# Performance work log

Measured on AMD Instinct MI355X. Metric: run time of the kernel, lower is better.

The kernel has to match this reference:

```python
import jax, jax.numpy as jnp
import numpy as np

NUM_HEADS = 12
HEAD_DIM = 64  # d_out // num_heads = 768 // 12


def setup_inputs() -> dict:
    key = jax.random.key(0)
    k1, k2 = jax.random.split(key)
    x = jax.random.normal(k1, (2, 2048, 768), dtype=jnp.float32)
    # torch Linear weight: [d_out, d_in], y = x @ W.T
    Wq = jax.random.normal(k2, (768, 768), dtype=jnp.float32) * 0.02
    return {"x": x, "Wq": Wq}


def reference(x, Wq):
    b, n, d_in = x.shape
    H, hd = NUM_HEADS, HEAD_DIM
    d_out = H * hd
    # NOTE: the original module uses Wq for queries, keys AND values.
    qkv = x @ Wq.T                                   # [b, n, d_out]
    h = qkv.reshape(b, n, H, hd).transpose(0, 2, 1, 3)  # [b, H, n, hd]
    scores = jnp.einsum('bhqd,bhkd->bhqk', h, h)      # [b, H, n, n]
    causal = jnp.triu(jnp.ones((n, n), dtype=bool), k=1)
    scores = jnp.where(causal, -jnp.inf, scores)
    attn = jax.nn.softmax(scores / jnp.sqrt(jnp.float32(hd)), axis=-1)
    ctx = jnp.einsum('bhqk,bhkd->bhqd', attn, h)      # [b, H, n, hd]
    # faithful to source: transpose(-2,-1) -> [b, H, hd, n], then view(b, n, d_out)
    ctx = ctx.transpose(0, 1, 3, 2)
    return ctx.reshape(b, n, d_out)
```

## Files before the change

### kernel.cpp

```cpp
#include <hip/hip_runtime.h>
#include <hip/hip_bf16.h>
#include <math.h>

typedef __attribute__((ext_vector_type(8))) short  short8;
typedef __attribute__((ext_vector_type(4))) float  floatx4;

#define MFMA16(a, b, c) __builtin_amdgcn_mfma_f32_16x16x32_bf16(a, b, c, 0, 0, 0)

constexpr int NSEQ = 2048;
constexpr int DIN  = 768;
constexpr int NH   = 12;
constexpr float QSCALE = 0.18033688011112042f;
constexpr int PART_STRIDE = 64 * 64 + 64;
constexpr size_t HB_ELEMS = (size_t)2 * NH * NSEQ * 64;

__device__ __forceinline__ ushort f2bf(float f) {
    unsigned u = __float_as_uint(f);
    u += 0x7FFF + ((u >> 16) & 1);
    return (ushort)(u >> 16);
}
__device__ __forceinline__ float bf2f(ushort u) {
    return __uint_as_float(((unsigned)u) << 16);
}
__device__ __forceinline__ unsigned pk2(float a, float b) {
    __hip_bfloat162 h = __float22bfloat162_rn(float2{a, b});
    return *(unsigned*)&h;
}
__device__ __forceinline__ short8 cvt8(float4 a, float4 b) {
    union { short8 s; unsigned u[4]; } r;
    r.u[0] = pk2(a.x, a.y); r.u[1] = pk2(a.z, a.w);
    r.u[2] = pk2(b.x, b.y); r.u[3] = pk2(b.z, b.w);
    return r.s;
}

__global__ __launch_bounds__(256, 3)
void qkv_mfma(const float* __restrict__ x, const float* __restrict__ Wq,
              ushort* __restrict__ h)
{
    __shared__ ushort As[64 * 72];
    __shared__ ushort Bs[128 * 72];

    const int tid  = threadIdx.x;
    const int w    = tid >> 6;
    const int lane = tid & 63;
    const int m    = lane & 15;
    const int quad = lane >> 4;
    const int r0   = blockIdx.x * 64;
    const int c0   = blockIdx.y * 128;
    const int mrow0 = (w & 1) * 32;
    const int ncol0 = (w >> 1) * 64;

    const int xr = tid >> 2, xc = (tid & 3) * 16;
    const int wr = tid >> 1, wc = (tid & 1) * 32;

    floatx4 C[2][4] = {};
    float4 xa[4], wa[8];

    #pragma unroll
    for (int j = 0; j < 4; ++j)
        xa[j] = *(const float4*)(x + (size_t)(r0 + xr) * DIN + xc + j * 4);
    #pragma unroll
    for (int j = 0; j < 8; ++j)
        wa[j] = *(const float4*)(Wq + (size_t)(c0 + wr) * DIN + wc + j * 4);

    for (int kk = 0; kk < 12; ++kk) {
        __syncthreads();
        *(short8*)&As[xr * 72 + xc]     = cvt8(xa[0], xa[1]);
        *(short8*)&As[xr * 72 + xc + 8] = cvt8(xa[2], xa[3]);
        #pragma unroll
        for (int v = 0; v < 4; ++v)
            *(short8*)&Bs[wr * 72 + wc + v * 8] = cvt8(wa[v * 2], wa[v * 2 + 1]);
        if (kk < 11) {
            const int k0 = (kk + 1) * 64;
            #pragma unroll
            for (int j = 0; j < 4; ++j)
                xa[j] = *(const float4*)(x + (size_t)(r0 + xr) * DIN + k0 + xc + j * 4);
            #pragma unroll
            for (int j = 0; j < 8; ++j)
                wa[j] = *(const float4*)(Wq + (size_t)(c0 + wr) * DIN + k0 + wc + j * 4);
        }
        __syncthreads();

        #pragma unroll
        for (int kt2 = 0; kt2 < 2; ++kt2) {
            short8 a0 = *(const short8*)&As[(mrow0 + m)      * 72 + kt2 * 32 + quad * 8];
            short8 a1 = *(const short8*)&As[(mrow0 + 16 + m) * 72 + kt2 * 32 + quad * 8];
            #pragma unroll
            for (int nt = 0; nt < 4; ++nt) {
                short8 bf = *(const short8*)&Bs[(ncol0 + nt * 16 + m) * 72 + kt2 * 32 + quad * 8];
                C[0][nt] = MFMA16(a0, bf, C[0][nt]);
                C[1][nt] = MFMA16(a1, bf, C[1][nt]);
            }
        }
    }

    #pragma unroll
    for (int mt = 0; mt < 2; ++mt)
        #pragma unroll
        for (int nt = 0; nt < 4; ++nt) {
            int cg = c0 + ncol0 + nt * 16 + m;
            int head = cg >> 6, d = cg & 63;
            #pragma unroll
            for (int r = 0; r < 4; ++r) {
                int rg = r0 + mrow0 + mt * 16 + quad * 4 + r;
                int b = rg >> 11, q = rg & 2047;
                h[((size_t)(b * NH + head) * NSEQ + q) * 64 + d] = f2bf(C[mt][nt][r]);
            }
        }
}

__global__ __launch_bounds__(256, 4)
void attn_mfma(const ushort* __restrict__ h, float* __restrict__ parts,
               float* __restrict__ out)
{
    __shared__ ushort Ks[64 * 72];
    __shared__ ushort Vt[80 * 72];
    __shared__ ushort Ps[4 * 16 * 72];

    const int tid  = threadIdx.x;
    const int w    = tid >> 6;
    const int lane = tid & 63;
    const int m    = lane & 15;
    const int quad = lane >> 4;

    const int u  = blockIdx.x;
    const int bh = blockIdx.y;
    int qt, kc;
    if (u < 32)      { qt = 24 + (u >> 2); kc = u & 3; }
    else if (u < 56) { int v = u - 32; int q3 = v / 3; qt = 16 + q3; kc = v - q3 * 3; }
    else if (u < 72) { int v = u - 56; qt = 8 + (v >> 1); kc = v & 1; }
    else             { qt = u - 72; kc = 0; }
    const int nc  = (qt + 8) >> 3;
    const int kt0 = kc * 8;
    const int kt1 = min(kc * 8 + 8, qt + 1);
    const int q0  = qt * 64;
    const int wq  = q0 + w * 16;
    const ushort* __restrict__ Hh = h + (size_t)bh * NSEQ * 64;

    if (tid < 32) ((unsigned*)&Vt[64 * 72])[tid] = 0x3F803F80u;

    short8 qa[2];
    #pragma unroll
    for (int kt2 = 0; kt2 < 2; ++kt2) {
        short8 raw = *(const short8*)(Hh + (size_t)(wq + m) * 64 + kt2 * 32 + quad * 8);
        #pragma unroll
        for (int j = 0; j < 8; ++j)
            qa[kt2][j] = (short)f2bf(bf2f((ushort)raw[j]) * QSCALE);
    }

    floatx4 O[4] = {};
    floatx4 O5 = {};
    ushort* Psw = Ps + w * 16 * 72;

    const int kr2  = (tid & 31) * 2;
    const int part = tid >> 5;

    short8 a0, a1;
    {
        const ushort* src = Hh + (size_t)(kt0 * 64 + kr2) * 64 + part * 8;
        a0 = *(const short8*)src;
        a1 = *(const short8*)(src + 64);
    }

    for (int kt = kt0; kt < kt1; ++kt) {
        __syncthreads();
        union { short8 v; ushort u[8]; } ua, ub;
        ua.v = a0; ub.v = a1;
        *(short8*)&Ks[kr2       * 72 + part * 8] = a0;
        *(short8*)&Ks[(kr2 + 1) * 72 + part * 8] = a1;
        #pragma unroll
        for (int i = 0; i < 8; ++i) {
            unsigned pk = (unsigned)ua.u[i] | ((unsigned)ub.u[i] << 16);
            *(unsigned*)&Vt[(part * 8 + i) * 72 + kr2] = pk;
        }
        if (kt + 1 < kt1) {
            const ushort* src = Hh + (size_t)((kt + 1) * 64 + kr2) * 64 + part * 8;
            a0 = *(const short8*)src;
            a1 = *(const short8*)(src + 64);
        }
        __syncthreads();

        floatx4 S[4] = {};
        #pragma unroll
        for (int kt2 = 0; kt2 < 2; ++kt2)
            #pragma unroll
            for (int mt = 0; mt < 4; ++mt) {
                short8 ka = *(const short8*)&Ks[(mt * 16 + m) * 72 + kt2 * 32 + quad * 8];
                S[mt] = MFMA16(ka, qa[kt2], S[mt]);
            }

        const int kb = kt * 64;
        if (kt == qt) {
            #pragma unroll
            for (int mt = 0; mt < 4; ++mt) {
                float p[4];
                #pragma unroll
                for (int r = 0; r < 4; ++r) {
                    int kg = kb + mt * 16 + quad * 4 + r;
                    p[r] = (kg <= wq + m) ? __builtin_amdgcn_exp2f(S[mt][r]) : 0.0f;
                }
                uint2 pw = {pk2(p[0], p[1]), pk2(p[2], p[3])};
                *(uint2*)&Psw[m * 72 + mt * 16 + quad * 4] = pw;
            }
        } else {
            #pragma unroll
            for (int mt = 0; mt < 4; ++mt) {
                float p[4];
                #pragma unroll
                for (int r = 0; r < 4; ++r)
                    p[r] = __builtin_amdgcn_exp2f(S[mt][r]);
                uint2 pw = {pk2(p[0], p[1]), pk2(p[2], p[3])};
                *(uint2*)&Psw[m * 72 + mt * 16 + quad * 4] = pw;
            }
        }

        #pragma unroll
        for (int kt2 = 0; kt2 < 2; ++kt2) {
            short8 pb = *(const short8*)&Psw[m * 72 + kt2 * 32 + quad * 8];
            #pragma unroll
            for (int mt = 0; mt < 4; ++mt) {
                short8 va = *(const short8*)&Vt[(mt * 16 + m) * 72 + kt2 * 32 + quad * 8];
                O[mt] = MFMA16(va, pb, O[mt]);
            }
            short8 v5 = *(const short8*)&Vt[(64 + m) * 72 + kt2 * 32 + quad * 8];
            O5 = MFMA16(v5, pb, O5);
        }
    }

    float lval = __shfl(O5[0], m);

    if (nc == 1) {
        float linv = 1.0f / lval;
        #pragma unroll
        for (int mt = 0; mt < 4; ++mt)
            #pragma unroll
            for (int r = 0; r < 4; ++r) {
                int d = mt * 16 + quad * 4 + r;
                out[((size_t)bh * 64 + d) * NSEQ + q0 + w * 16 + m] = O[mt][r] * linv;
            }
    } else {
        float* P = parts + (size_t)((bh * 32 + qt) * 4 + kc) * PART_STRIDE;
        #pragma unroll
        for (int mt = 0; mt < 4; ++mt)
            #pragma unroll
            for (int r = 0; r < 4; ++r)
                P[(mt * 16 + quad * 4 + r) * 64 + w * 16 + m] = O[mt][r];
        if (quad == 0) P[4096 + w * 16 + m] = O5[0];
    }
}

__global__ __launch_bounds__(256)
void combine(const float* __restrict__ parts, float* __restrict__ out)
{
    const int qt = 8 + blockIdx.x;
    const int bh = blockIdx.y;
    const int nc = (qt + 8) >> 3;
    const float* base = parts + (size_t)((bh * 32 + qt) * 4) * PART_STRIDE;

    __shared__ float linv[64];
    const int tid = threadIdx.x;
    if (tid < 64) {
        float s = 0.0f;
        for (int c = 0; c < nc; ++c) s += base[c * PART_STRIDE + 4096 + tid];
        linv[tid] = 1.0f / s;
    }
    __syncthreads();

    const int d  = tid >> 2;
    const int qo = (tid & 3) * 16;
    float4 acc[4] = {};
    for (int c = 0; c < nc; ++c) {
        const float4* p = (const float4*)(base + c * PART_STRIDE + d * 64 + qo);
        #pragma unroll
        for (int j = 0; j < 4; ++j) {
            float4 v = p[j];
            acc[j].x += v.x; acc[j].y += v.y; acc[j].z += v.z; acc[j].w += v.w;
        }
    }
    float* dst = out + ((size_t)bh * 64 + d) * NSEQ + qt * 64 + qo;
    #pragma unroll
    for (int j = 0; j < 4; ++j) {
        float4 lv = *(const float4*)&linv[qo + j * 4];
        float4 o = make_float4(acc[j].x * lv.x, acc[j].y * lv.y,
                               acc[j].z * lv.z, acc[j].w * lv.w);
        *(float4*)(dst + j * 4) = o;
    }
}

extern "C" void kernel_launch(void* const* d_in, const int* in_sizes, int n_in,
                              void* d_out, int out_size, void* d_ws, size_t ws_size,
                              hipStream_t stream)
{
    (void)in_sizes; (void)n_in; (void)out_size; (void)ws_size;
    const float* x  = (const float*)d_in[0];
    const float* Wq = (const float*)d_in[1];
    float* out = (float*)d_out;

    ushort* hb    = (ushort*)d_ws;
    float*  partb = (float*)((char*)d_ws + HB_ELEMS * sizeof(ushort));

    qkv_mfma<<<dim3(64, 6),  dim3(256), 0, stream>>>(x, Wq, hb);
    attn_mfma<<<dim3(80, 24), dim3(256), 0, stream>>>(hb, partb, out);
    combine<<<dim3(24, 24),  dim3(256), 0, stream>>>(partb, out);
}
```

Measured before the change: 136.7 us.

## Fuse split-K combine into attention kernel via last-block atomic counter

```diff
diff --git a/kernel.cpp b/kernel.cpp
--- a/kernel.cpp
+++ b/kernel.cpp
@@ -12,7 +12,9 @@
 constexpr int NH   = 12;
 constexpr float QSCALE = 0.18033688011112042f;
 constexpr int PART_STRIDE = 64 * 64 + 64;
+constexpr int NSTRIPS = 24 * 32;
 constexpr size_t HB_ELEMS = (size_t)2 * NH * NSEQ * 64;
+constexpr size_t PARTS_ELEMS = (size_t)NSTRIPS * 4 * PART_STRIDE;
 
 __device__ __forceinline__ ushort f2bf(float f) {
     unsigned u = __float_as_uint(f);
@@ -35,12 +37,15 @@
 
 __global__ __launch_bounds__(256, 3)
 void qkv_mfma(const float* __restrict__ x, const float* __restrict__ Wq,
-              ushort* __restrict__ h)
+              ushort* __restrict__ h, int* __restrict__ cnt)
 {
     __shared__ ushort As[64 * 72];
     __shared__ ushort Bs[128 * 72];
 
     const int tid  = threadIdx.x;
+    if (blockIdx.x == 0 && blockIdx.y == 0)
+        for (int i = tid; i < NSTRIPS; i += 256) cnt[i] = 0;
+
     const int w    = tid >> 6;
     const int lane = tid & 63;
     const int m    = lane & 15;
@@ -111,11 +116,13 @@
 
 __global__ __launch_bounds__(256, 4)
 void attn_mfma(const ushort* __restrict__ h, float* __restrict__ parts,
-               float* __restrict__ out)
+               int* __restrict__ cnt, float* __restrict__ out)
 {
     __shared__ ushort Ks[64 * 72];
     __shared__ ushort Vt[80 * 72];
     __shared__ ushort Ps[4 * 16 * 72];
+    __shared__ float  linvS[64];
+    __shared__ int    lastFlag;
 
     const int tid  = threadIdx.x;
     const int w    = tid >> 6;
@@ -238,31 +245,32 @@
                 int d = mt * 16 + quad * 4 + r;
                 out[((size_t)bh * 64 + d) * NSEQ + q0 + w * 16 + m] = O[mt][r] * linv;
             }
-    } else {
-        float* P = parts + (size_t)((bh * 32 + qt) * 4 + kc) * PART_STRIDE;
-        #pragma unroll
-        for (int mt = 0; mt < 4; ++mt)
-            #pragma unroll
-            for (int r = 0; r < 4; ++r)
-                P[(mt * 16 + quad * 4 + r) * 64 + w * 16 + m] = O[mt][r];
-        if (quad == 0) P[4096 + w * 16 + m] = O5[0];
-    }
-}
-
-__global__ __launch_bounds__(256)
-void combine(const float* __restrict__ parts, float* __restrict__ out)
-{
-    const int qt = 8 + blockIdx.x;
-    const int bh = blockIdx.y;
-    const int nc = (qt + 8) >> 3;
-    const float* base = parts + (size_t)((bh * 32 + qt) * 4) * PART_STRIDE;
-
-    __shared__ float linv[64];
-    const int tid = threadIdx.x;
+        return;
+    }
+
+    const size_t strip = (size_t)(bh * 32 + qt);
+    float* P = parts + (strip * 4 + kc) * PART_STRIDE;
+    #pragma unroll
+    for (int mt = 0; mt < 4; ++mt)
+        #pragma unroll
+        for (int r = 0; r < 4; ++r)
+            P[(mt * 16 + quad * 4 + r) * 64 + w * 16 + m] = O[mt][r];
+    if (quad == 0) P[4096 + w * 16 + m] = O5[0];
+
+    __threadfence();
+    if (tid == 0) {
+        int old = atomicAdd(&cnt[strip], 1);
+        lastFlag = (old == nc - 1);
+    }
+    __syncthreads();
+    if (!lastFlag) return;
+    __threadfence();
+
+    const float* base = parts + strip * 4 * PART_STRIDE;
     if (tid < 64) {
         float s = 0.0f;
         for (int c = 0; c < nc; ++c) s += base[c * PART_STRIDE + 4096 + tid];
-        linv[tid] = 1.0f / s;
+        linvS[tid] = 1.0f / s;
     }
     __syncthreads();
 
@@ -277,13 +285,12 @@
             acc[j].x += v.x; acc[j].y += v.y; acc[j].z += v.z; acc[j].w += v.w;
         }
     }
-    float* dst = out + ((size_t)bh * 64 + d) * NSEQ + qt * 64 + qo;
+    float* dst = out + ((size_t)bh * 64 + d) * NSEQ + q0 + qo;
     #pragma unroll
     for (int j = 0; j < 4; ++j) {
-        float4 lv = *(const float4*)&linv[qo + j * 4];
-        float4 o = make_float4(acc[j].x * lv.x, acc[j].y * lv.y,
-                               acc[j].z * lv.z, acc[j].w * lv.w);
-        *(float4*)(dst + j * 4) = o;
+        float4 lv = *(const float4*)&linvS[qo + j * 4];
+        *(float4*)(dst + j * 4) = make_float4(acc[j].x * lv.x, acc[j].y * lv.y,
+                                              acc[j].z * lv.z, acc[j].w * lv.w);
     }
 }
 
@@ -298,8 +305,8 @@
 
     ushort* hb    = (ushort*)d_ws;
     float*  partb = (float*)((char*)d_ws + HB_ELEMS * sizeof(ushort));
-
-    qkv_mfma<<<dim3(64, 6),  dim3(256), 0, stream>>>(x, Wq, hb);
-    attn_mfma<<<dim3(80, 24), dim3(256), 0, stream>>>(hb, partb, out);
-    combine<<<dim3(24, 24),  dim3(256), 0, stream>>>(partb, out);
-}
+    int*    cntb  = (int*)(partb + PARTS_ELEMS);
+
+    qkv_mfma<<<dim3(64, 6),  dim3(256), 0, stream>>>(x, Wq, hb, cntb);
+    attn_mfma<<<dim3(80, 24), dim3(256), 0, stream>>>(hb, partb, cntb, out);
+}
```

Measured after the change: 474.2 us. +246.8%, slower.
